# Optimization experiments

Measured on AMD Instinct MI355X. Metric: run time of the kernel, lower is better.

Reference implementation:

```python
import jax, jax.numpy as jnp
import numpy as np

B, IN, HID, OUT = 1024, 256, 512, 2
MU_INIT, LOGVAR_INIT = 0.0, -5.0
VAR_MIN = 1e-6


def setup_inputs() -> dict:
    key = jax.random.key(0)
    ks = jax.random.split(key, 9)
    inp = {
        "x": jax.random.normal(ks[0], (B, IN), dtype=jnp.float32),
        "w1_mu": MU_INIT + 0.1 * jax.random.normal(ks[1], (HID, IN), dtype=jnp.float32),
        "w1_logvar": LOGVAR_INIT + 0.1 * jax.random.normal(ks[2], (HID, IN), dtype=jnp.float32),
        "b1_mu": MU_INIT + 0.1 * jax.random.normal(ks[3], (HID,), dtype=jnp.float32),
        "b1_logvar": LOGVAR_INIT + 0.1 * jax.random.normal(ks[4], (HID,), dtype=jnp.float32),
        "w2_mu": MU_INIT + 0.1 * jax.random.normal(ks[5], (OUT, HID), dtype=jnp.float32),
        "w2_logvar": LOGVAR_INIT + 0.1 * jax.random.normal(ks[6], (OUT, HID), dtype=jnp.float32),
        "b2_mu": MU_INIT + 0.1 * jax.random.normal(ks[7], (OUT,), dtype=jnp.float32),
        "b2_logvar": LOGVAR_INIT + 0.1 * jax.random.normal(ks[8], (OUT,), dtype=jnp.float32),
    }
    return inp


def _bayes_linear(x, w_mu, w_logvar, b_mu, b_logvar, eps_w, eps_b):
    # Non-efficient path: per-example sampled weights (batch, out, in) and biases (batch, out)
    w_std = jnp.exp(0.5 * w_logvar)
    b_std = jnp.exp(0.5 * b_logvar)
    weights = w_mu[None, :, :] + w_std[None, :, :] * eps_w  # (B, O, I)
    biases = b_mu[None, :] + b_std[None, :] * eps_b          # (B, O)
    out = jnp.einsum("boi,bi->bo", weights, x)
    return out + biases


def reference(x, w1_mu, w1_logvar, b1_mu, b1_logvar, w2_mu, w2_logvar, b2_mu, b2_logvar):
    # Noise sampled inside forward, matching torch.randn in the module (fixed key for determinism)
    nk = jax.random.split(jax.random.key(42), 4)
    eps_w1 = jax.random.normal(nk[0], (B, HID, IN), dtype=x.dtype)
    eps_b1 = jax.random.normal(nk[1], (B, HID), dtype=x.dtype)
    eps_w2 = jax.random.normal(nk[2], (B, OUT, HID), dtype=x.dtype)
    eps_b2 = jax.random.normal(nk[3], (B, OUT), dtype=x.dtype)

    h = jax.nn.relu(_bayes_linear(x, w1_mu, w1_logvar, b1_mu, b1_logvar, eps_w1, eps_b1))
    out = _bayes_linear(h, w2_mu, w2_logvar, b2_mu, b2_logvar, eps_w2, eps_b2)  # (B, 2)
    mean = out[:, 0]
    var = jnp.maximum(jnp.exp(out[:, 1]), VAR_MIN)
    return mean, var
```

## Files before the change

### kernel.cpp

```cpp
#include <hip/hip_runtime.h>
#include <stdint.h>

#define BATCH 1024
#define IN    256
#define HID   512
#define OUT   2

#define HALF_W2 524288u
#define HALF_B2 1024u

__host__ __device__ __forceinline__ uint32_t rotl32(uint32_t x, uint32_t r) {
#ifdef __HIP_DEVICE_COMPILE__
    return __builtin_rotateleft32(x, r);
#else
    return (x << r) | (x >> (32 - r));
#endif
}

__host__ __device__ __forceinline__ void threefry2x32(uint32_t k0, uint32_t k1,
                                                      uint32_t& x0, uint32_t& x1) {
    uint32_t k2 = k0 ^ k1 ^ 0x1BD11BDAu;
    x0 += k0; x1 += k1;
#define TF_R(r) { x0 += x1; x1 = rotl32(x1, (r)); x1 ^= x0; }
    TF_R(13) TF_R(15) TF_R(26) TF_R(6)   x0 += k1; x1 += k2 + 1u;
    TF_R(17) TF_R(29) TF_R(16) TF_R(24)  x0 += k2; x1 += k0 + 2u;
    TF_R(13) TF_R(15) TF_R(26) TF_R(6)   x0 += k0; x1 += k1 + 3u;
    TF_R(17) TF_R(29) TF_R(16) TF_R(24)  x0 += k1; x1 += k2 + 4u;
    TF_R(13) TF_R(15) TF_R(26) TF_R(6)   x0 += k2; x1 += k0 + 5u;
#undef TF_R
}

__device__ __forceinline__ uint32_t tf_bits(uint32_t k0, uint32_t k1, uint32_t cnt) {
    uint32_t x0 = 0u, x1 = cnt;
    threefry2x32(k0, k1, x0, x1);
    return x0 ^ x1;
}

__device__ __forceinline__ float bits_to_normal(uint32_t bits) {
    const float LO = -0.99999994f;
    float f = __uint_as_float((bits >> 9) | 0x3f800000u) - 1.0f;
    float u = fmaxf(LO, fmaf(f, 2.0f, LO));
    float w = -__logf(fmaf(-u, u, 1.0f));
    float p;
    if (w < 5.0f) {
        w -= 2.5f;
        p = 2.81022636e-08f;
        p = fmaf(p, w, 3.43273939e-07f);
        p = fmaf(p, w, -3.5233877e-06f);
        p = fmaf(p, w, -4.39150654e-06f);
        p = fmaf(p, w, 0.00021858087f);
        p = fmaf(p, w, -0.00125372503f);
        p = fmaf(p, w, -0.00417768164f);
        p = fmaf(p, w, 0.246640727f);
        p = fmaf(p, w, 1.50140941f);
    } else {
        w = __fsqrt_rn(w) - 3.0f;
        p = -0.000200214257f;
        p = fmaf(p, w, 0.000100950558f);
        p = fmaf(p, w, 0.00134934322f);
        p = fmaf(p, w, -0.00367342844f);
        p = fmaf(p, w, 0.00573950773f);
        p = fmaf(p, w, -0.0076224613f);
        p = fmaf(p, w, 0.00943887047f);
        p = fmaf(p, w, 1.00167406f);
        p = fmaf(p, w, 2.83297682f);
    }
    return 1.41421356f * p * u;
}

__global__ __launch_bounds__(256) void k_w1std(const float* __restrict__ w1_logvar,
                                               float* __restrict__ w1_std) {
    int i = blockIdx.x * 256 + threadIdx.x;
    if (i < HID * IN) w1_std[i] = __expf(0.5f * w1_logvar[i]);
}

__global__ __launch_bounds__(256, 4) void k_layer1(
    const float* __restrict__ x, const float* __restrict__ w1_mu,
    const float* __restrict__ w1_std, const float* __restrict__ b1_mu,
    const float* __restrict__ b1_logvar, float* __restrict__ h,
    uint32_t kw0, uint32_t kw1, uint32_t kb0, uint32_t kb1)
{
    __shared__ float xs[IN];
    const int b = blockIdx.y;
    const int o = blockIdx.x * 256 + threadIdx.x;
    xs[threadIdx.x] = x[b * IN + threadIdx.x];
    __syncthreads();

    const float4* wm4 = (const float4*)(w1_mu  + o * IN);
    const float4* ws4 = (const float4*)(w1_std + o * IN);
    const float4* x4  = (const float4*)xs;

    uint32_t c = (uint32_t)(b * HID + o) * IN;

    float acc = 0.f;
    #pragma unroll 2
    for (int i4 = 0; i4 < IN / 4; ++i4) {
        float4 m4 = wm4[i4], s4 = ws4[i4], xv = x4[i4];
        float e0 = bits_to_normal(tf_bits(kw0, kw1, c));
        float e1 = bits_to_normal(tf_bits(kw0, kw1, c + 1u));
        float e2 = bits_to_normal(tf_bits(kw0, kw1, c + 2u));
        float e3 = bits_to_normal(tf_bits(kw0, kw1, c + 3u));
        c += 4u;
        acc = fmaf(fmaf(s4.x, e0, m4.x), xv.x, acc);
        acc = fmaf(fmaf(s4.y, e1, m4.y), xv.y, acc);
        acc = fmaf(fmaf(s4.z, e2, m4.z), xv.z, acc);
        acc = fmaf(fmaf(s4.w, e3, m4.w), xv.w, acc);
    }
    float eb = bits_to_normal(tf_bits(kb0, kb1, (uint32_t)(b * HID + o)));
    float hv = acc + fmaf(__expf(0.5f * b1_logvar[o]), eb, b1_mu[o]);
    h[b * HID + o] = fmaxf(hv, 0.f);
}

__global__ __launch_bounds__(256) void k_layer2(
    const float* __restrict__ h, const float* __restrict__ w2_mu,
    const float* __restrict__ w2_logvar, const float* __restrict__ b2_mu,
    const float* __restrict__ b2_logvar, float* __restrict__ out,
    uint32_t kw0, uint32_t kw1, uint32_t kb0, uint32_t kb1)
{
    const int wave = (blockIdx.x * 256 + threadIdx.x) >> 6;
    const int lane = threadIdx.x & 63;
    const int b = wave >> 1, j = wave & 1;

    float acc0 = 0.f, acc1 = 0.f;
    #pragma unroll
    for (int oi = 0; oi < HID / 64; ++oi) {
        int o = oi * 64 + lane;
        uint32_t c = (uint32_t)((b * OUT + j) * HID + o);
        float e0 = bits_to_normal(tf_bits(kw0, kw1, c));
        float e1 = bits_to_normal(tf_bits(kw0, kw1, c + HALF_W2));
        float m = w2_mu[j * HID + o];
        float s = __expf(0.5f * w2_logvar[j * HID + o]);
        acc0 = fmaf(fmaf(s, e0, m), h[b * HID + o], acc0);
        acc1 = fmaf(fmaf(s, e1, m), h[(b + 512) * HID + o], acc1);
    }
    #pragma unroll
    for (int off = 32; off > 0; off >>= 1) {
        acc0 += __shfl_down(acc0, off, 64);
        acc1 += __shfl_down(acc1, off, 64);
    }
    if (lane == 0) {
        uint32_t cb = (uint32_t)(b * OUT + j);
        float eb0 = bits_to_normal(tf_bits(kb0, kb1, cb));
        float eb1 = bits_to_normal(tf_bits(kb0, kb1, cb + HALF_B2));
        float bstd = __expf(0.5f * b2_logvar[j]);
        float bm = b2_mu[j];
        float o0 = acc0 + fmaf(bstd, eb0, bm);
        float o1 = acc1 + fmaf(bstd, eb1, bm);
        if (j == 0) {
            out[b] = o0;
            out[b + 512] = o1;
        } else {
            out[1024 + b]       = fmaxf(__expf(o0), 1e-6f);
            out[1024 + b + 512] = fmaxf(__expf(o1), 1e-6f);
        }
    }
}

extern "C" void kernel_launch(void* const* d_in, const int* in_sizes, int n_in,
                              void* d_out, int out_size, void* d_ws, size_t ws_size,
                              hipStream_t stream) {
    (void)in_sizes; (void)n_in; (void)out_size; (void)ws_size;
    const float* x         = (const float*)d_in[0];
    const float* w1_mu     = (const float*)d_in[1];
    const float* w1_logvar = (const float*)d_in[2];
    const float* b1_mu     = (const float*)d_in[3];
    const float* b1_logvar = (const float*)d_in[4];
    const float* w2_mu     = (const float*)d_in[5];
    const float* w2_logvar = (const float*)d_in[6];
    const float* b2_mu     = (const float*)d_in[7];
    const float* b2_logvar = (const float*)d_in[8];
    float* out = (float*)d_out;

    float* ws_w1std = (float*)d_ws;
    float* ws_h     = (float*)d_ws + HID * IN;

    uint32_t nk[4][2];
    for (uint32_t i = 0; i < 4; ++i) {
        uint32_t a = 0u, c = i;
        threefry2x32(0u, 42u, a, c);
        nk[i][0] = a; nk[i][1] = c;
    }
    const uint32_t kw1a = nk[0][0], kw1b = nk[0][1];
    const uint32_t kb1a = nk[1][0], kb1b = nk[1][1];
    const uint32_t kw2a = nk[2][0], kw2b = nk[2][1];
    const uint32_t kb2a = nk[3][0], kb2b = nk[3][1];

    k_w1std<<<(HID * IN + 255) / 256, 256, 0, stream>>>(w1_logvar, ws_w1std);
    k_layer1<<<dim3(2, 1024), 256, 0, stream>>>(x, w1_mu, ws_w1std, b1_mu, b1_logvar,
                                                ws_h, kw1a, kw1b, kb1a, kb1b);
    k_layer2<<<256, 256, 0, stream>>>(ws_h, w2_mu, w2_logvar, b2_mu, b2_logvar,
                                      out, kw2a, kw2b, kb2a, kb2b);
}
```

Before: 372.2 us.

## Precompute Threefry key schedule, fold constants into erfinv, prefetch layer1 loads

Hoists the Threefry key-schedule sums into a per-thread struct and simplifies the first round for a zero x0 input, which trims integer ops per random draw. The inverse-erf normal conversion now uses log2 directly, folds sqrt(2) into the polynomial coefficients and merges the mantissa-to-uniform step into one FMA. The layer-1 loop is software-pipelined so the next weight and x loads are issued before the current RNG work, with the unroll factor raised. This targets the ALU-bound RNG cost, at the price of more registers and small floating-point rounding differences.

Result: faster. 346.5 us (-6.9%).

```diff
diff --git a/kernel.cpp b/kernel.cpp
--- a/kernel.cpp
+++ b/kernel.cpp
@@ -8,6 +8,8 @@
 
 #define HALF_W2 524288u
 #define HALF_B2 1024u
+
+#define SQRT2 1.4142135623730951
 
 __host__ __device__ __forceinline__ uint32_t rotl32(uint32_t x, uint32_t r) {
 #ifdef __HIP_DEVICE_COMPILE__
@@ -30,42 +32,73 @@
 #undef TF_R
 }
 
-__device__ __forceinline__ uint32_t tf_bits(uint32_t k0, uint32_t k1, uint32_t cnt) {
-    uint32_t x0 = 0u, x1 = cnt;
-    threefry2x32(k0, k1, x0, x1);
-    return x0 ^ x1;
+struct TFK {
+    uint32_t k0, k1, k2, K01, i1b, i2b, i3b, i4b, i5b;
+    __device__ __forceinline__ TFK(uint32_t a, uint32_t b) {
+        k0 = a; k1 = b; k2 = a ^ b ^ 0x1BD11BDAu;
+        K01 = k0 + k1;
+        i1b = k2 + 1u; i2b = k0 + 2u; i3b = k1 + 3u; i4b = k2 + 4u; i5b = k0 + 5u;
+    }
+};
+
+__device__ __forceinline__ uint32_t tf_bits(const TFK& K, uint32_t cnt) {
+    uint32_t t  = cnt + K.k1;
+    uint32_t x0 = cnt + K.K01;
+    uint32_t x1 = rotl32(t, 13) ^ x0;
+    x0 += x1; x1 = rotl32(x1, 15) ^ x0;
+    x0 += x1; x1 = rotl32(x1, 26) ^ x0;
+    x0 += x1; x1 = rotl32(x1,  6) ^ x0;
+    t = x1 + K.i1b; x0 = x0 + t + K.k1;  x1 = rotl32(t, 17) ^ x0;
+    x0 += x1; x1 = rotl32(x1, 29) ^ x0;
+    x0 += x1; x1 = rotl32(x1, 16) ^ x0;
+    x0 += x1; x1 = rotl32(x1, 24) ^ x0;
+    t = x1 + K.i2b; x0 = x0 + t + K.k2;  x1 = rotl32(t, 13) ^ x0;
+    x0 += x1; x1 = rotl32(x1, 15) ^ x0;
+    x0 += x1; x1 = rotl32(x1, 26) ^ x0;
+    x0 += x1; x1 = rotl32(x1,  6) ^ x0;
+    t = x1 + K.i3b; x0 = x0 + t + K.k0;  x1 = rotl32(t, 17) ^ x0;
+    x0 += x1; x1 = rotl32(x1, 29) ^ x0;
+    x0 += x1; x1 = rotl32(x1, 16) ^ x0;
+    x0 += x1; x1 = rotl32(x1, 24) ^ x0;
+    t = x1 + K.i4b; x0 = x0 + t + K.k1;  x1 = rotl32(t, 13) ^ x0;
+    x0 += x1; x1 = rotl32(x1, 15) ^ x0;
+    x0 += x1; x1 = rotl32(x1, 26) ^ x0;
+    x0 += x1; x1 = rotl32(x1,  6) ^ x0;
+    return (x0 + K.k2) ^ (x1 + K.i5b);
 }
 
 __device__ __forceinline__ float bits_to_normal(uint32_t bits) {
     const float LO = -0.99999994f;
-    float f = __uint_as_float((bits >> 9) | 0x3f800000u) - 1.0f;
-    float u = fmaxf(LO, fmaf(f, 2.0f, LO));
-    float w = -__logf(fmaf(-u, u, 1.0f));
+    float m = __uint_as_float((bits >> 9) | 0x3f800000u);
+    float u = fmaxf(LO, fmaf(m, 2.0f, -3.0f));
+    float z = fmaf(-u, u, 1.0f);
+    float L = __log2f(z);
     float p;
-    if (w < 5.0f) {
-        w -= 2.5f;
-        p = 2.81022636e-08f;
-        p = fmaf(p, w, 3.43273939e-07f);
-        p = fmaf(p, w, -3.5233877e-06f);
-        p = fmaf(p, w, -4.39150654e-06f);
-        p = fmaf(p, w, 0.00021858087f);
-        p = fmaf(p, w, -0.00125372503f);
-        p = fmaf(p, w, -0.00417768164f);
-        p = fmaf(p, w, 0.246640727f);
-        p = fmaf(p, w, 1.50140941f);
+    if (L > -7.2134752f) {
+        float wa = fmaf(L, -0.69314718f, -2.5f);
+        p = (float)(2.81022636e-08 * SQRT2);
+        p = fmaf(p, wa, (float)(3.43273939e-07 * SQRT2));
+        p = fmaf(p, wa, (float)(-3.5233877e-06 * SQRT2));
+        p = fmaf(p, wa, (float)(-4.39150654e-06 * SQRT2));
+        p = fmaf(p, wa, (float)(0.00021858087 * SQRT2));
+        p = fmaf(p, wa, (float)(-0.00125372503 * SQRT2));
+        p = fmaf(p, wa, (float)(-0.00417768164 * SQRT2));
+        p = fmaf(p, wa, (float)(0.246640727 * SQRT2));
+        p = fmaf(p, wa, (float)(1.50140941 * SQRT2));
     } else {
-        w = __fsqrt_rn(w) - 3.0f;
-        p = -0.000200214257f;
-        p = fmaf(p, w, 0.000100950558f);
-        p = fmaf(p, w, 0.00134934322f);
-        p = fmaf(p, w, -0.00367342844f);
-        p = fmaf(p, w, 0.00573950773f);
-        p = fmaf(p, w, -0.0076224613f);
-        p = fmaf(p, w, 0.00943887047f);
-        p = fmaf(p, w, 1.00167406f);
-        p = fmaf(p, w, 2.83297682f);
-    }
-    return 1.41421356f * p * u;
+        float w = L * -0.69314718f;
+        float wb = __fsqrt_rn(w) - 3.0f;
+        p = (float)(-0.000200214257 * SQRT2);
+        p = fmaf(p, wb, (float)(0.000100950558 * SQRT2));
+        p = fmaf(p, wb, (float)(0.00134934322 * SQRT2));
+        p = fmaf(p, wb, (float)(-0.00367342844 * SQRT2));
+        p = fmaf(p, wb, (float)(0.00573950773 * SQRT2));
+        p = fmaf(p, wb, (float)(-0.0076224613 * SQRT2));
+        p = fmaf(p, wb, (float)(0.00943887047 * SQRT2));
+        p = fmaf(p, wb, (float)(1.00167406 * SQRT2));
+        p = fmaf(p, wb, (float)(2.83297682 * SQRT2));
+    }
+    return p * u;
 }
 
 __global__ __launch_bounds__(256) void k_w1std(const float* __restrict__ w1_logvar,
@@ -86,27 +119,41 @@
     xs[threadIdx.x] = x[b * IN + threadIdx.x];
     __syncthreads();
 
+    const TFK Kw(kw0, kw1);
     const float4* wm4 = (const float4*)(w1_mu  + o * IN);
     const float4* ws4 = (const float4*)(w1_std + o * IN);
     const float4* x4  = (const float4*)xs;
 
     uint32_t c = (uint32_t)(b * HID + o) * IN;
-
     float acc = 0.f;
-    #pragma unroll 2
-    for (int i4 = 0; i4 < IN / 4; ++i4) {
-        float4 m4 = wm4[i4], s4 = ws4[i4], xv = x4[i4];
-        float e0 = bits_to_normal(tf_bits(kw0, kw1, c));
-        float e1 = bits_to_normal(tf_bits(kw0, kw1, c + 1u));
-        float e2 = bits_to_normal(tf_bits(kw0, kw1, c + 2u));
-        float e3 = bits_to_normal(tf_bits(kw0, kw1, c + 3u));
+
+    float4 m4 = wm4[0], s4 = ws4[0], xv = x4[0];
+    #pragma unroll 3
+    for (int i4 = 0; i4 < IN / 4 - 1; ++i4) {
+        float4 m4n = wm4[i4 + 1], s4n = ws4[i4 + 1], xvn = x4[i4 + 1];
+        float e0 = bits_to_normal(tf_bits(Kw, c));
+        float e1 = bits_to_normal(tf_bits(Kw, c + 1u));
+        float e2 = bits_to_normal(tf_bits(Kw, c + 2u));
+        float e3 = bits_to_normal(tf_bits(Kw, c + 3u));
         c += 4u;
         acc = fmaf(fmaf(s4.x, e0, m4.x), xv.x, acc);
         acc = fmaf(fmaf(s4.y, e1, m4.y), xv.y, acc);
         acc = fmaf(fmaf(s4.z, e2, m4.z), xv.z, acc);
         acc = fmaf(fmaf(s4.w, e3, m4.w), xv.w, acc);
-    }
-    float eb = bits_to_normal(tf_bits(kb0, kb1, (uint32_t)(b * HID + o)));
+        m4 = m4n; s4 = s4n; xv = xvn;
+    }
+    {
+        float e0 = bits_to_normal(tf_bits(Kw, c));
+        float e1 = bits_to_normal(tf_bits(Kw, c + 1u));
+        float e2 = bits_to_normal(tf_bits(Kw, c + 2u));
+        float e3 = bits_to_normal(tf_bits(Kw, c + 3u));
+        acc = fmaf(fmaf(s4.x, e0, m4.x), xv.x, acc);
+        acc = fmaf(fmaf(s4.y, e1, m4.y), xv.y, acc);
+        acc = fmaf(fmaf(s4.z, e2, m4.z), xv.z, acc);
+        acc = fmaf(fmaf(s4.w, e3, m4.w), xv.w, acc);
+    }
+    const TFK Kb(kb0, kb1);
+    float eb = bits_to_normal(tf_bits(Kb, (uint32_t)(b * HID + o)));
     float hv = acc + fmaf(__expf(0.5f * b1_logvar[o]), eb, b1_mu[o]);
     h[b * HID + o] = fmaxf(hv, 0.f);
 }
@@ -120,14 +167,15 @@
     const int wave = (blockIdx.x * 256 + threadIdx.x) >> 6;
     const int lane = threadIdx.x & 63;
     const int b = wave >> 1, j = wave & 1;
+    const TFK Kw(kw0, kw1);
 
     float acc0 = 0.f, acc1 = 0.f;
     #pragma unroll
     for (int oi = 0; oi < HID / 64; ++oi) {
         int o = oi * 64 + lane;
         uint32_t c = (uint32_t)((b * OUT + j) * HID + o);
-        float e0 = bits_to_normal(tf_bits(kw0, kw1, c));
-        float e1 = bits_to_normal(tf_bits(kw0, kw1, c + HALF_W2));
+        float e0 = bits_to_normal(tf_bits(Kw, c));
+        float e1 = bits_to_normal(tf_bits(Kw, c + HALF_W2));
         float m = w2_mu[j * HID + o];
         float s = __expf(0.5f * w2_logvar[j * HID + o]);
         acc0 = fmaf(fmaf(s, e0, m), h[b * HID + o], acc0);
@@ -139,9 +187,10 @@
         acc1 += __shfl_down(acc1, off, 64);
     }
     if (lane == 0) {
+        const TFK Kb(kb0, kb1);
         uint32_t cb = (uint32_t)(b * OUT + j);
-        float eb0 = bits_to_normal(tf_bits(kb0, kb1, cb));
-        float eb1 = bits_to_normal(tf_bits(kb0, kb1, cb + HALF_B2));
+        float eb0 = bits_to_normal(tf_bits(Kb, cb));
+        float eb1 = bits_to_normal(tf_bits(Kb, cb + HALF_B2));
         float bstd = __expf(0.5f * b2_logvar[j]);
         float bm = b2_mu[j];
         float o0 = acc0 + fmaf(bstd, eb0, bm);
```
